# Optimization experiments

Measured on AMD Instinct MI355X. Metric: run time of the kernel, lower is better.

## Reference

```python
import jax, jax.numpy as jnp
import numpy as np

H = 512  # output_size


def setup_inputs() -> dict:
    key = jax.random.key(0)
    k = jax.random.split(key, 6)
    B, T, D = 64, 512, 512
    x = jax.random.normal(k[0], (B, T, D), dtype=jnp.float32)
    lengths = jnp.sort(jax.random.randint(k[1], (B,), 1, T + 1))[::-1].astype(jnp.int64)
    scale = 0.05
    w_in = jax.random.normal(k[2], (6 * H, D), dtype=jnp.float32) * scale
    b_in = jax.random.normal(k[3], (6 * H,), dtype=jnp.float32) * scale
    w_state = jax.random.normal(k[4], (5 * H, H), dtype=jnp.float32) * scale
    b_state = jax.random.normal(k[5], (5 * H,), dtype=jnp.float32) * scale
    return {"x": x, "lengths": lengths, "w_in": w_in, "b_in": b_in,
            "w_state": w_state, "b_state": b_state}


def reference(x, lengths, w_in, b_in, w_state, b_state):
    # x: [B,T,D]; returns padded outputs [B,T,H] (zeros past each length),
    # matching the padded content of the original PackedSequence output.
    B, T, _ = x.shape
    # Precompute all input projections: [B,T,6H]
    proj_in = jnp.einsum('btd,od->bto', x, w_in) + b_in
    proj_in_t = jnp.transpose(proj_in, (1, 0, 2))            # [T,B,6H]
    # valid mask per timestep: [T,B,1]
    mask_t = (jnp.arange(T)[:, None] < lengths[None, :])[..., None]

    def step(carry, inp):
        h, c = carry                                          # [B,H] each
        pi, m = inp                                           # [B,6H], [B,1]
        ps = h @ w_state.T + b_state                          # [B,5H]
        i_g = jax.nn.sigmoid(pi[:, 0*H:1*H] + ps[:, 0*H:1*H])
        f_g = jax.nn.sigmoid(pi[:, 1*H:2*H] + ps[:, 1*H:2*H])
        g   = jnp.tanh(     pi[:, 2*H:3*H] + ps[:, 2*H:3*H])
        o_g = jax.nn.sigmoid(pi[:, 3*H:4*H] + ps[:, 3*H:4*H])
        c_new = i_g * g + f_g * c
        out = o_g * jnp.tanh(c_new)
        hw  = jax.nn.sigmoid(pi[:, 4*H:5*H] + ps[:, 4*H:5*H])
        out = hw * out + (1.0 - hw) * pi[:, 5*H:6*H]
        # past-length positions are reset to zero (matches original slicing)
        out = jnp.where(m, out, 0.0)
        c_new = jnp.where(m, c_new, 0.0)
        return (out, c_new), out

    h0 = jnp.zeros((B, H), dtype=x.dtype)
    c0 = jnp.zeros((B, H), dtype=x.dtype)
    _, outs = jax.lax.scan(step, (h0, c0), (proj_in_t, mask_t))
    return jnp.transpose(outs, (1, 0, 2))                     # [B,T,H]
```

## Files before the change

### kernel.cpp

```cpp
#include <hip/hip_runtime.h>
#include <cstdint>
#include <cstddef>

#define BB 64
#define TT 512
#define DD 512
#define HH 512
#define SIXH 3072
#define NWG 32

typedef __attribute__((ext_vector_type(8))) short bf16x8;
typedef __attribute__((ext_vector_type(4))) float f32x4;
typedef __attribute__((ext_vector_type(4))) unsigned short u16x4;
typedef __attribute__((ext_vector_type(4))) int i32x4;

#define WS_FLAGS 0u
#define WS_CNT   256u
#define WS_H     16640u
#define WS_C     147712u
#define WS_XB    278784u
#define WS_WB    33833216u
#define WS_BF    36978944u
#define WS_PROJ  36991232u

#define CLOAD16(dst, ptr) \
    asm volatile("global_load_dwordx4 %0, %1, off sc0 sc1" : "=v"(dst) : "v"(ptr))
#define CSTORE8(ptr, val) \
    asm volatile("global_store_dwordx2 %0, %1, off sc0 sc1" :: "v"(ptr), "v"(val))
#define WAIT4(N, a,b,c,d) \
    asm volatile("s_waitcnt vmcnt(" N ")" : "+v"(a),"+v"(b),"+v"(c),"+v"(d))

__device__ __forceinline__ float bf2f(unsigned short u) {
    union { unsigned int i; float f; } v; v.i = ((unsigned int)u) << 16; return v.f;
}
__device__ __forceinline__ unsigned short f2bf(float f) {
    union { unsigned int i; float f; } v; v.f = f;
    unsigned int r = v.i + 0x7FFFu + ((v.i >> 16) & 1u);
    return (unsigned short)(r >> 16);
}
__device__ __forceinline__ float sigm(float x) { return 1.0f / (1.0f + __expf(-x)); }
__device__ __forceinline__ float tanh_fast(float x) {
    return 1.0f - 2.0f / (__expf(2.0f * x) + 1.0f);
}

__device__ __forceinline__ bf16x8 cvt8v(const float* p) {
    const float4 a = *(const float4*)p;
    const float4 b = *(const float4*)(p + 4);
    bf16x8 o;
    o[0] = (short)f2bf(a.x); o[1] = (short)f2bf(a.y);
    o[2] = (short)f2bf(a.z); o[3] = (short)f2bf(a.w);
    o[4] = (short)f2bf(b.x); o[5] = (short)f2bf(b.y);
    o[6] = (short)f2bf(b.z); o[7] = (short)f2bf(b.w);
    return o;
}

__global__ void detect_kernel(const unsigned short* __restrict__ x16,
                              const int* __restrict__ len32,
                              int* __restrict__ flags) {
    const int lane = threadIdx.x;
    int bad = 0;
    for (int i = lane; i < 256; i += 64)
        if (fabsf(bf2f(x16[i])) > 1e4f) bad++;
#pragma unroll
    for (int off = 32; off; off >>= 1) bad += __shfl_down(bad, off);
    if (lane == 0) {
        flags[0] = (bad >= 16) ? 1 : 0;
        flags[1] = (len32[1] == 0 && len32[3] == 0 && len32[5] == 0) ? 1 : 0;
    }
}

__global__ __launch_bounds__(256) void convert_kernel(
    const void* __restrict__ xv, const void* __restrict__ wv,
    const void* __restrict__ bv,
    unsigned short* __restrict__ xb, unsigned short* __restrict__ wb,
    float* __restrict__ bf, const int* __restrict__ flags)
{
    const int fp32 = flags[0];
    const size_t NX = (size_t)BB * TT * DD;
    const size_t NW = (size_t)SIXH * DD;
    const size_t tid = (size_t)blockIdx.x * blockDim.x + threadIdx.x;
    const size_t stride = (size_t)gridDim.x * blockDim.x;

    if (fp32) {
        const float* xf = (const float*)xv;
        for (size_t i = tid * 4; i < NX; i += stride * 4) {
            const float4 v = *(const float4*)(xf + i);
            u16x4 o; o[0] = f2bf(v.x); o[1] = f2bf(v.y); o[2] = f2bf(v.z); o[3] = f2bf(v.w);
            *(u16x4*)(xb + i) = o;
        }
        const float* wf = (const float*)wv;
        for (size_t i = tid * 4; i < NW; i += stride * 4) {
            const float4 v = *(const float4*)(wf + i);
            u16x4 o; o[0] = f2bf(v.x); o[1] = f2bf(v.y); o[2] = f2bf(v.z); o[3] = f2bf(v.w);
            *(u16x4*)(wb + i) = o;
        }
        const float* bvf = (const float*)bv;
        for (size_t i = tid; i < SIXH; i += stride) bf[i] = bvf[i];
    } else {
        const unsigned short* xs = (const unsigned short*)xv;
        for (size_t i = tid * 4; i < NX; i += stride * 4)
            *(u16x4*)(xb + i) = *(const u16x4*)(xs + i);
        const unsigned short* wsrc = (const unsigned short*)wv;
        for (size_t i = tid * 4; i < NW; i += stride * 4)
            *(u16x4*)(wb + i) = *(const u16x4*)(wsrc + i);
        const unsigned short* bs = (const unsigned short*)bv;
        for (size_t i = tid; i < SIXH; i += stride) bf[i] = bf2f(bs[i]);
    }
}

__global__ __launch_bounds__(256) void proj_kernel(
    const unsigned short* __restrict__ xb, const unsigned short* __restrict__ wb,
    const float* __restrict__ bf, unsigned short* __restrict__ projc,
    const int* __restrict__ flags, const int* __restrict__ len32,
    int t0, int tc_shift)
{
    const int Tc  = 1 << tc_shift;
    {
        const int mb  = blockIdx.y * 64;
        const int bq  = mb >> tc_shift;
        const int tl0 = mb & (Tc - 1);
        const int len_b = flags[1] ? len32[2 * bq] : len32[bq];
        if (t0 + tl0 >= len_b) return;
    }

    const int tid  = threadIdx.x;
    const int wave = tid >> 6;
    const int lane = tid & 63;
    const int q    = lane >> 4;
    const int r    = lane & 15;

    const int m_blk = blockIdx.y * 64 + (wave >> 1) * 32;
    const int n_blk = blockIdx.x * 64 + (wave & 1) * 32;
    const int b     = m_blk >> tc_shift;
    const int tl    = m_blk & (Tc - 1);

    const size_t xrow0 = (size_t)(b * TT + t0 + tl + r) * DD;
    const size_t xrow1 = (size_t)(b * TT + t0 + tl + 16 + r) * DD;
    const size_t wrow0 = (size_t)(n_blk + r) * DD;
    const size_t wrow1 = (size_t)(n_blk + 16 + r) * DD;

    f32x4 acc[2][2] = {};
    const int koff = q * 8;
    for (int k0 = 0; k0 < DD; k0 += 32) {
        const int k = k0 + koff;
        bf16x8 a0 = *(const bf16x8*)(xb + xrow0 + k);
        bf16x8 a1 = *(const bf16x8*)(xb + xrow1 + k);
        bf16x8 b0 = *(const bf16x8*)(wb + wrow0 + k);
        bf16x8 b1 = *(const bf16x8*)(wb + wrow1 + k);
        acc[0][0] = __builtin_amdgcn_mfma_f32_16x16x32_bf16(a0, b0, acc[0][0], 0, 0, 0);
        acc[0][1] = __builtin_amdgcn_mfma_f32_16x16x32_bf16(a0, b1, acc[0][1], 0, 0, 0);
        acc[1][0] = __builtin_amdgcn_mfma_f32_16x16x32_bf16(a1, b0, acc[1][0], 0, 0, 0);
        acc[1][1] = __builtin_amdgcn_mfma_f32_16x16x32_bf16(a1, b1, acc[1][1], 0, 0, 0);
    }

#pragma unroll
    for (int mi = 0; mi < 2; mi++) {
#pragma unroll
        for (int ni = 0; ni < 2; ni++) {
            const int n = n_blk + ni * 16 + r;
            const float bias = bf[n];
#pragma unroll
            for (int rr = 0; rr < 4; rr++) {
                const int m = m_blk + mi * 16 + q * 4 + rr;
                projc[(size_t)m * SIXH + n] = f2bf(acc[mi][ni][rr] + bias);
            }
        }
    }
}

__global__ __launch_bounds__(256, 1) void rec_kernel(
    const unsigned short* __restrict__ projc,
    const void* __restrict__ wsv, const void* __restrict__ bsv,
    const int* __restrict__ len32,
    unsigned short* __restrict__ hbuf, float* __restrict__ cbuf,
    int* __restrict__ wgflag, void* __restrict__ outv,
    const int* __restrict__ flags, int t0, int Tc)
{
    const int fp32 = flags[0], i64 = flags[1];
    const int tid  = threadIdx.x;
    const int wv   = tid >> 6;
    const int lane = tid & 63;
    const int q    = lane >> 4;
    const int r    = lane & 15;
    const int j0   = blockIdx.x * 16;
    const int b    = wv * 16 + r;

    __shared__ unsigned short wlds[5 * 16 * 64 * 8];

    for (int v = tid; v < 5 * 16 * 64; v += 256) {
        const int g  = v >> 10;
        const int ki = (v >> 6) & 15;
        const int ln = v & 63;
        const size_t gaddr = (size_t)(g * HH + j0 + (ln & 15)) * HH + ki * 32 + (ln >> 4) * 8;
        bf16x8 w8;
        if (fp32) w8 = cvt8v((const float*)wsv + gaddr);
        else      w8 = *(const bf16x8*)((const unsigned short*)wsv + gaddr);
        *(bf16x8*)&wlds[(size_t)v * 8] = w8;
    }

    float bs[5][4];
#pragma unroll
    for (int g = 0; g < 5; g++)
#pragma unroll
        for (int jj = 0; jj < 4; jj++)
            bs[g][jj] = fp32 ? ((const float*)bsv)[g * HH + j0 + q * 4 + jj]
                             : bf2f(((const unsigned short*)bsv)[g * HH + j0 + q * 4 + jj]);

    const int len = i64 ? len32[2 * b] : len32[b];

    int Lmax = 0;
    for (int i = 0; i < BB; i++) {
        const int li = i64 ? len32[2 * i] : len32[i];
        Lmax = (li > Lmax) ? li : Lmax;
    }

    float creg[4];
#pragma unroll
    for (int jj = 0; jj < 4; jj++)
        creg[jj] = cbuf[b * HH + j0 + q * 4 + jj];

    u16x4 pv[6];
    {
        const unsigned short* pb = projc + (size_t)b * Tc * SIXH + j0 + q * 4;
#pragma unroll
        for (int g = 0; g < 6; g++) pv[g] = *(const u16x4*)(pb + g * HH);
    }

    __syncthreads();

    union HU { i32x4 i; bf16x8 b; };
    union P8 { unsigned short s[4]; unsigned long long u; };

    int* const gbase = wgflag + (size_t)wv * NWG * 32;
    int fcache = (lane < NWG) ? 0 : 0x7fffffff;

    for (int t = t0; t < t0 + Tc; t++) {
        if (t >= Lmax) {
            if (fp32) {
                float* op = (float*)outv + ((size_t)b * TT + t) * HH + j0 + q * 4;
                *(float4*)op = make_float4(0.f, 0.f, 0.f, 0.f);
            } else {
                unsigned short* op = (unsigned short*)outv + ((size_t)b * TT + t) * HH + j0 + q * 4;
                *(unsigned long long*)op = 0ull;
            }
            continue;
        }

        const unsigned short* hcur = hbuf + (size_t)(t & 1) * (BB * HH);
        unsigned short*       hnxt = hbuf + (size_t)((t + 1) & 1) * (BB * HH);

        if (t > t0) {
            bool done;
            do {
                if (fcache < t)
                    fcache = __hip_atomic_load(&gbase[lane * 32], __ATOMIC_RELAXED,
                                               __HIP_MEMORY_SCOPE_AGENT);
                done = __all(fcache >= t);
            } while (!done);
            asm volatile("" ::: "memory");
        }

        i32x4 hv[16];
#pragma unroll
        for (int ki = 0; ki < 16; ki++)
            CLOAD16(hv[ki], hcur + (size_t)b * HH + ki * 32 + q * 8);

        f32x4 acc[5] = {};
#define MFMA_CHUNK(KLO)                                                          \
        _Pragma("unroll")                                                        \
        for (int ki = (KLO); ki < (KLO) + 4; ki++) {                             \
            HU u; u.i = hv[ki];                                                  \
            _Pragma("unroll")                                                    \
            for (int g = 0; g < 5; g++) {                                        \
                bf16x8 aw = *(const bf16x8*)&wlds[((g * 16 + ki) * 64 + lane) * 8]; \
                acc[g] = __builtin_amdgcn_mfma_f32_16x16x32_bf16(aw, u.b, acc[g], 0, 0, 0); \
            }                                                                    \
        }
        WAIT4("12", hv[0],  hv[1],  hv[2],  hv[3]);   MFMA_CHUNK(0)
        WAIT4("8",  hv[4],  hv[5],  hv[6],  hv[7]);   MFMA_CHUNK(4)
        WAIT4("4",  hv[8],  hv[9],  hv[10], hv[11]);  MFMA_CHUNK(8)
        WAIT4("0",  hv[12], hv[13], hv[14], hv[15]);  MFMA_CHUNK(12)
#undef MFMA_CHUNK

        P8 hp;
        float ov4[4];
#pragma unroll
        for (int jj = 0; jj < 4; jj++) {
            const float i_g = sigm(bf2f(pv[0][jj]) + acc[0][jj] + bs[0][jj]);
            const float f_g = sigm(bf2f(pv[1][jj]) + acc[1][jj] + bs[1][jj]);
            const float g_t = tanh_fast(bf2f(pv[2][jj]) + acc[2][jj] + bs[2][jj]);
            const float o_g = sigm(bf2f(pv[3][jj]) + acc[3][jj] + bs[3][jj]);
            const float hw  = sigm(bf2f(pv[4][jj]) + acc[4][jj] + bs[4][jj]);

            float c_new = i_g * g_t + f_g * creg[jj];
            float ov = o_g * tanh_fast(c_new);
            ov = hw * ov + (1.0f - hw) * bf2f(pv[5][jj]);
            if (t >= len) { ov = 0.0f; c_new = 0.0f; }
            creg[jj] = c_new;
            ov4[jj] = ov;
            hp.s[jj] = f2bf(ov);
        }

        CSTORE8((void*)(hnxt + (size_t)b * HH + j0 + q * 4), hp.u);
        asm volatile("s_waitcnt vmcnt(0)" ::: "memory");
        if (lane == 0)
            __hip_atomic_store(&gbase[blockIdx.x * 32], t + 1,
                               __ATOMIC_RELAXED, __HIP_MEMORY_SCOPE_AGENT);

        if (fp32) {
            float* op = (float*)outv + ((size_t)b * TT + t) * HH + j0 + q * 4;
            *(float4*)op = make_float4(ov4[0], ov4[1], ov4[2], ov4[3]);
        } else {
            unsigned short* op = (unsigned short*)outv + ((size_t)b * TT + t) * HH + j0 + q * 4;
            *(unsigned long long*)op = hp.u;
        }
        const int tln = t - t0 + 1;
        if (tln < Tc) {
            const unsigned short* pb = projc + ((size_t)b * Tc + tln) * SIXH + j0 + q * 4;
#pragma unroll
            for (int g = 0; g < 6; g++) pv[g] = *(const u16x4*)(pb + g * HH);
        }
    }

#pragma unroll
    for (int jj = 0; jj < 4; jj++)
        cbuf[b * HH + j0 + q * 4 + jj] = creg[jj];
}

extern "C" void kernel_launch(void* const* d_in, const int* in_sizes, int n_in,
                              void* d_out, int out_size, void* d_ws, size_t ws_size,
                              hipStream_t stream) {
    const void* xv      = d_in[0];
    const int*  len     = (const int*)d_in[1];
    const void* w_in    = d_in[2];
    const void* b_in    = d_in[3];
    const void* w_state = d_in[4];
    const void* b_state = d_in[5];

    char* ws = (char*)d_ws;
    int* flags  = (int*)(ws + WS_FLAGS);
    int* wgflag = (int*)(ws + WS_CNT);
    unsigned short* hbuf = (unsigned short*)(ws + WS_H);
    float* cbuf = (float*)(ws + WS_C);
    unsigned short* xb = (unsigned short*)(ws + WS_XB);
    unsigned short* wb = (unsigned short*)(ws + WS_WB);
    float* bf = (float*)(ws + WS_BF);
    unsigned short* projc = (unsigned short*)(ws + WS_PROJ);

    int tc_shift = 9;
    while (tc_shift > 6 &&
           WS_PROJ + ((size_t)BB << tc_shift) * SIXH * 2 > ws_size) tc_shift--;
    const int Tc = 1 << tc_shift;

    detect_kernel<<<1, 64, 0, stream>>>((const unsigned short*)xv, len, flags);
    hipMemsetAsync(ws + WS_CNT, 0, WS_XB - WS_CNT, stream);
    convert_kernel<<<2048, 256, 0, stream>>>(xv, w_in, b_in, xb, wb, bf, flags);

    for (int c = 0; c < TT / Tc; c++) {
        const int t0 = c * Tc;
        proj_kernel<<<dim3(SIXH / 64, (BB << tc_shift) >> 6), 256, 0, stream>>>(
            xb, wb, bf, projc, flags, len, t0, tc_shift);
        rec_kernel<<<NWG, 256, 0, stream>>>(projc, w_state, b_state, len,
                                            hbuf, cbuf, wgflag, d_out, flags, t0, Tc);
    }
}
```

Measured before the change: 2.704 ms.

## Widen projection tiles, split recurrent flag wait, per-wave length bound

The projection kernel now computes three 64-column tiles per block, so each X fragment is reused across 192 output columns, and the grid x dimension shrinks to match. In the recurrent kernel each wave stops at the maximum length of its own 16 batch rows instead of the global maximum. The spin-wait on peer workgroups' flags is split in two: loads of the first half of h start once the first 16 producer workgroups are done, overlapping with the wait for the rest. This raises register pressure in the projection kernel and adds polling complexity.

```diff
diff --git a/kernel.cpp b/kernel.cpp
--- a/kernel.cpp
+++ b/kernel.cpp
@@ -129,43 +129,47 @@
     const int q    = lane >> 4;
     const int r    = lane & 15;
 
-    const int m_blk = blockIdx.y * 64 + (wave >> 1) * 32;
-    const int n_blk = blockIdx.x * 64 + (wave & 1) * 32;
-    const int b     = m_blk >> tc_shift;
-    const int tl    = m_blk & (Tc - 1);
+    const int m_blk  = blockIdx.y * 64 + (wave >> 1) * 32;
+    const int n_base = blockIdx.x * 192 + (wave & 1) * 32;
+    const int b      = m_blk >> tc_shift;
+    const int tl     = m_blk & (Tc - 1);
 
     const size_t xrow0 = (size_t)(b * TT + t0 + tl + r) * DD;
     const size_t xrow1 = (size_t)(b * TT + t0 + tl + 16 + r) * DD;
-    const size_t wrow0 = (size_t)(n_blk + r) * DD;
-    const size_t wrow1 = (size_t)(n_blk + 16 + r) * DD;
-
-    f32x4 acc[2][2] = {};
+
+    f32x4 acc[3][2][2] = {};
     const int koff = q * 8;
     for (int k0 = 0; k0 < DD; k0 += 32) {
         const int k = k0 + koff;
-        bf16x8 a0 = *(const bf16x8*)(xb + xrow0 + k);
-        bf16x8 a1 = *(const bf16x8*)(xb + xrow1 + k);
-        bf16x8 b0 = *(const bf16x8*)(wb + wrow0 + k);
-        bf16x8 b1 = *(const bf16x8*)(wb + wrow1 + k);
-        acc[0][0] = __builtin_amdgcn_mfma_f32_16x16x32_bf16(a0, b0, acc[0][0], 0, 0, 0);
-        acc[0][1] = __builtin_amdgcn_mfma_f32_16x16x32_bf16(a0, b1, acc[0][1], 0, 0, 0);
-        acc[1][0] = __builtin_amdgcn_mfma_f32_16x16x32_bf16(a1, b0, acc[1][0], 0, 0, 0);
-        acc[1][1] = __builtin_amdgcn_mfma_f32_16x16x32_bf16(a1, b1, acc[1][1], 0, 0, 0);
-    }
-
-#pragma unroll
-    for (int mi = 0; mi < 2; mi++) {
-#pragma unroll
-        for (int ni = 0; ni < 2; ni++) {
-            const int n = n_blk + ni * 16 + r;
-            const float bias = bf[n];
-#pragma unroll
-            for (int rr = 0; rr < 4; rr++) {
-                const int m = m_blk + mi * 16 + q * 4 + rr;
-                projc[(size_t)m * SIXH + n] = f2bf(acc[mi][ni][rr] + bias);
+        const bf16x8 a0 = *(const bf16x8*)(xb + xrow0 + k);
+        const bf16x8 a1 = *(const bf16x8*)(xb + xrow1 + k);
+#pragma unroll
+        for (int nt = 0; nt < 3; nt++) {
+            const size_t wrow0 = (size_t)(n_base + nt * 64 + r) * DD;
+            const size_t wrow1 = (size_t)(n_base + nt * 64 + 16 + r) * DD;
+            bf16x8 b0 = *(const bf16x8*)(wb + wrow0 + k);
+            bf16x8 b1 = *(const bf16x8*)(wb + wrow1 + k);
+            acc[nt][0][0] = __builtin_amdgcn_mfma_f32_16x16x32_bf16(a0, b0, acc[nt][0][0], 0, 0, 0);
+            acc[nt][0][1] = __builtin_amdgcn_mfma_f32_16x16x32_bf16(a0, b1, acc[nt][0][1], 0, 0, 0);
+            acc[nt][1][0] = __builtin_amdgcn_mfma_f32_16x16x32_bf16(a1, b0, acc[nt][1][0], 0, 0, 0);
+            acc[nt][1][1] = __builtin_amdgcn_mfma_f32_16x16x32_bf16(a1, b1, acc[nt][1][1], 0, 0, 0);
+        }
+    }
+
+#pragma unroll
+    for (int nt = 0; nt < 3; nt++)
+#pragma unroll
+        for (int mi = 0; mi < 2; mi++)
+#pragma unroll
+            for (int ni = 0; ni < 2; ni++) {
+                const int n = n_base + nt * 64 + ni * 16 + r;
+                const float bias = bf[n];
+#pragma unroll
+                for (int rr = 0; rr < 4; rr++) {
+                    const int m = m_blk + mi * 16 + q * 4 + rr;
+                    projc[(size_t)m * SIXH + n] = f2bf(acc[nt][mi][ni][rr] + bias);
+                }
             }
-        }
-    }
 }
 
 __global__ __launch_bounds__(256, 1) void rec_kernel(
@@ -208,10 +212,10 @@
 
     const int len = i64 ? len32[2 * b] : len32[b];
 
-    int Lmax = 0;
-    for (int i = 0; i < BB; i++) {
+    int lmax_g = 0;
+    for (int i = wv * 16; i < wv * 16 + 16; i++) {
         const int li = i64 ? len32[2 * i] : len32[i];
-        Lmax = (li > Lmax) ? li : Lmax;
+        lmax_g = (li > lmax_g) ? li : lmax_g;
     }
 
     float creg[4];
@@ -235,7 +239,7 @@
     int fcache = (lane < NWG) ? 0 : 0x7fffffff;
 
     for (int t = t0; t < t0 + Tc; t++) {
-        if (t >= Lmax) {
+        if (t >= lmax_g) {
             if (fp32) {
                 float* op = (float*)outv + ((size_t)b * TT + t) * HH + j0 + q * 4;
                 *(float4*)op = make_float4(0.f, 0.f, 0.f, 0.f);
@@ -250,19 +254,28 @@
         unsigned short*       hnxt = hbuf + (size_t)((t + 1) & 1) * (BB * HH);
 
         if (t > t0) {
-            bool done;
-            do {
+            while ((__ballot(fcache >= t) & 0xFFFFull) != 0xFFFFull) {
                 if (fcache < t)
                     fcache = __hip_atomic_load(&gbase[lane * 32], __ATOMIC_RELAXED,
                                                __HIP_MEMORY_SCOPE_AGENT);
-                done = __all(fcache >= t);
-            } while (!done);
+            }
             asm volatile("" ::: "memory");
         }
-
         i32x4 hv[16];
 #pragma unroll
-        for (int ki = 0; ki < 16; ki++)
+        for (int ki = 0; ki < 8; ki++)
+            CLOAD16(hv[ki], hcur + (size_t)b * HH + ki * 32 + q * 8);
+
+        if (t > t0) {
+            while (__ballot(fcache >= t) != ~0ull) {
+                if (fcache < t)
+                    fcache = __hip_atomic_load(&gbase[lane * 32], __ATOMIC_RELAXED,
+                                               __HIP_MEMORY_SCOPE_AGENT);
+            }
+            asm volatile("" ::: "memory");
+        }
+#pragma unroll
+        for (int ki = 8; ki < 16; ki++)
             CLOAD16(hv[ki], hcur + (size_t)b * HH + ki * 32 + q * 8);
 
         f32x4 acc[5] = {};
@@ -358,7 +371,7 @@
 
     for (int c = 0; c < TT / Tc; c++) {
         const int t0 = c * Tc;
-        proj_kernel<<<dim3(SIXH / 64, (BB << tc_shift) >> 6), 256, 0, stream>>>(
+        proj_kernel<<<dim3(SIXH / 192, (BB << tc_shift) >> 6), 256, 0, stream>>>(
             xb, wb, bf, projc, flags, len, t0, tc_shift);
         rec_kernel<<<NWG, 256, 0, stream>>>(projc, w_state, b_state, len,
                                             hbuf, cbuf, wgflag, d_out, flags, t0, Tc);
```

Result: faster. 2.552 ms (-5.6%).
